# Performance work log

Measured on AMD Instinct MI355X. Metric: run time of the kernel, lower is better.

## Reference

```python
import jax, jax.numpy as jnp
import numpy as np

NUM_HEAD = 12
DIM_MODEL = 768
HEAD_DIM = DIM_MODEL // NUM_HEAD


def setup_inputs() -> dict:
    key = jax.random.key(0)
    ks = jax.random.split(key, 4)
    B, S, D = 2, 2048, DIM_MODEL
    scale = 1.0 / np.sqrt(D)
    return {
        "v1": jax.random.normal(ks[0], (B, S, D), dtype=jnp.float32),
        "v1_mask": jnp.zeros((B, 1, 1, S), dtype=jnp.float32),
        "Wq": jax.random.normal(ks[1], (D, D), dtype=jnp.float32) * scale,
        "bq": jnp.zeros((D,), dtype=jnp.float32),
        "Wk": jax.random.normal(ks[2], (D, D), dtype=jnp.float32) * scale,
        "bk": jnp.zeros((D,), dtype=jnp.float32),
        "Wv": jax.random.normal(ks[3], (D, D), dtype=jnp.float32) * scale,
        "bv": jnp.zeros((D,), dtype=jnp.float32),
    }


def reference(v1, v1_mask, Wq, bq, Wk, bk, Wv, bv):
    B, S, D = v1.shape
    H, hd = NUM_HEAD, HEAD_DIM

    def split_heads(x):  # [B,S,D] -> [B,H,S,hd]
        return x.reshape(B, S, H, hd).transpose(0, 2, 1, 3)

    q = split_heads(v1 @ Wq + bq)
    k = split_heads(v1 @ Wk + bk)
    v = split_heads(v1 @ Wv + bv)

    scores = jnp.einsum("bhqd,bhkd->bhqk", q, k) / jnp.sqrt(jnp.float32(hd))
    scores = scores + v1_mask  # additive mask broadcasts over heads/query
    probs = jax.nn.softmax(scores, axis=-1)
    # dropout is identity in eval/reference mode
    ctx = jnp.einsum("bhqk,bhkd->bhqd", probs, v)
    return ctx.transpose(0, 2, 1, 3).reshape(B, S, D)
```

## Files before the change

kernel.cpp:

```cpp
#include <hip/hip_runtime.h>
#include <math.h>

#define B_SZ 2
#define S_SZ 2048
#define D_SZ 768
#define NH   12
#define HD   64
#define BH_T (B_SZ * NH)
#define M_TOT (B_SZ * S_SZ)

using bfrag = __attribute__((ext_vector_type(8))) short;
using ffrag = __attribute__((ext_vector_type(4))) float;

__device__ __forceinline__ unsigned short f2bf(float f) {
    unsigned int u = __float_as_uint(f);
    u += 0x7fffu + ((u >> 16) & 1u);
    return (unsigned short)(u >> 16);
}
__device__ __forceinline__ unsigned short f2bf_fast(float f) {
    return (unsigned short)((__float_as_uint(f) + 0x8000u) >> 16);
}

__device__ __forceinline__ void async16(void* lds, const void* gp) {
    __builtin_amdgcn_global_load_lds(
        (const __attribute__((address_space(1))) unsigned int*)gp,
        (__attribute__((address_space(3))) unsigned int*)lds,
        16, 0, 0);
}

__global__ __launch_bounds__(256) void cvt_v1(const float* __restrict__ in,
                                              unsigned short* __restrict__ out) {
    int i = (blockIdx.x * 256 + threadIdx.x) * 4;
    float4 v = *(const float4*)&in[i];
    ushort4 o;
    o.x = f2bf(v.x); o.y = f2bf(v.y); o.z = f2bf(v.z); o.w = f2bf(v.w);
    *(ushort4*)&out[i] = o;
}

__global__ __launch_bounds__(256) void transpose_w(
    const float* __restrict__ Wq, const float* __restrict__ Wk,
    const float* __restrict__ Wv, unsigned short* __restrict__ Wt) {
    const int z = blockIdx.z;
    const float* W = (z == 0) ? Wq : (z == 1) ? Wk : Wv;
    unsigned short* dst = Wt + (size_t)z * D_SZ * D_SZ;
    __shared__ float tile[64][65];
    const int t = threadIdx.x;
    const int n0 = blockIdx.x * 64, k0 = blockIdx.y * 64;
    #pragma unroll
    for (int i = 0; i < 16; ++i) {
        int flat = i * 256 + t;
        int r = flat >> 6, c = flat & 63;
        tile[r][c] = W[(size_t)(k0 + r) * D_SZ + n0 + c];
    }
    __syncthreads();
    #pragma unroll
    for (int i = 0; i < 16; ++i) {
        int flat = i * 256 + t;
        int r = flat >> 6, c = flat & 63;
        dst[(size_t)(n0 + r) * D_SZ + k0 + c] = f2bf(tile[c][r]);
    }
}

#define CP_LD 136

__global__ __launch_bounds__(256) void proj_gemm(
    const unsigned short* __restrict__ Ab,
    const unsigned short* __restrict__ Wt,
    const float* __restrict__ bq, const float* __restrict__ bk_,
    const float* __restrict__ bv_,
    unsigned short* __restrict__ Qb, unsigned short* __restrict__ Kb,
    unsigned short* __restrict__ Vtb) {
    const int z = blockIdx.z;
    const unsigned short* Bt = Wt + (size_t)z * D_SZ * D_SZ;
    const float* bias = (z == 0) ? bq : (z == 1) ? bk_ : bv_;

    __shared__ unsigned short smem[128 * CP_LD];
    unsigned short* As = smem;
    unsigned short* Bs = smem + 128 * 64;

    const int t = threadIdx.x;
    const int lane = t & 63;
    const int w = t >> 6;
    const int wm = w & 1, wn = w >> 1;
    const int col = lane & 15;
    const int quad = lane >> 4;
    const int m0 = blockIdx.y * 128;
    const int n0 = blockIdx.x * 128;
    const int wbase = t & ~63;

    ffrag acc[4][4];
    #pragma unroll
    for (int i = 0; i < 4; ++i)
        #pragma unroll
        for (int j = 0; j < 4; ++j) { ffrag zf = {0.f, 0.f, 0.f, 0.f}; acc[i][j] = zf; }

    for (int k0 = 0; k0 < D_SZ; k0 += 64) {
        __syncthreads();
        #pragma unroll
        for (int i = 0; i < 4; ++i) {
            int c = i * 256 + t;
            int row = c >> 3;
            int gcol = ((c & 7) ^ (row & 7)) * 8;
            async16(&As[(size_t)(i * 256 + wbase) * 8],
                    &Ab[(size_t)(m0 + row) * D_SZ + k0 + gcol]);
        }
        #pragma unroll
        for (int i = 0; i < 4; ++i) {
            int c = i * 256 + t;
            int row = c >> 3;
            int gcol = ((c & 7) ^ (row & 7)) * 8;
            async16(&Bs[(size_t)(i * 256 + wbase) * 8],
                    &Bt[(size_t)(n0 + row) * D_SZ + k0 + gcol]);
        }
        __syncthreads();
        #pragma unroll
        for (int kk = 0; kk < 64; kk += 32) {
            const int cc = (kk >> 3) + quad;
            bfrag a[4], b[4];
            #pragma unroll
            for (int mi = 0; mi < 4; ++mi) {
                int row = wm * 64 + mi * 16 + col;
                a[mi] = *(const bfrag*)&As[row * 64 + ((cc ^ (row & 7)) * 8)];
            }
            #pragma unroll
            for (int ni = 0; ni < 4; ++ni) {
                int row = wn * 64 + ni * 16 + col;
                b[ni] = *(const bfrag*)&Bs[row * 64 + ((cc ^ (row & 7)) * 8)];
            }
            if (z == 2) {
                #pragma unroll
                for (int mi = 0; mi < 4; ++mi)
                    #pragma unroll
                    for (int ni = 0; ni < 4; ++ni)
                        acc[mi][ni] = __builtin_amdgcn_mfma_f32_16x16x32_bf16(
                            a[mi], b[ni], acc[mi][ni], 0, 0, 0);
            } else {
                #pragma unroll
                for (int mi = 0; mi < 4; ++mi)
                    #pragma unroll
                    for (int ni = 0; ni < 4; ++ni)
                        acc[mi][ni] = __builtin_amdgcn_mfma_f32_16x16x32_bf16(
                            b[ni], a[mi], acc[mi][ni], 0, 0, 0);
            }
        }
    }

    __syncthreads();

    if (z < 2) {
        const float sc = (z == 0) ? 0.125f : 1.0f;
        #pragma unroll
        for (int mi = 0; mi < 4; ++mi) {
            int m_local = wm * 64 + mi * 16 + col;
            #pragma unroll
            for (int ni = 0; ni < 4; ++ni) {
                int n_base = wn * 64 + ni * 16 + quad * 4;
                float4 b4 = *(const float4*)&bias[n0 + n_base];
                uint2 pk;
                pk.x = (unsigned)f2bf((acc[mi][ni][0] + b4.x) * sc) |
                       ((unsigned)f2bf((acc[mi][ni][1] + b4.y) * sc) << 16);
                pk.y = (unsigned)f2bf((acc[mi][ni][2] + b4.z) * sc) |
                       ((unsigned)f2bf((acc[mi][ni][3] + b4.w) * sc) << 16);
                *(uint2*)&smem[m_local * CP_LD + n_base] = pk;
            }
        }
        __syncthreads();
        unsigned short* Out = (z == 0) ? Qb : Kb;
        #pragma unroll
        for (int j = 0; j < 8; ++j) {
            int flat = j * 256 + t;
            int row = flat >> 4;
            int ch = flat & 15;
            uint4 vv = *(const uint4*)&smem[row * CP_LD + ch * 8];
            int m = m0 + row;
            int bb = m >> 11, s = m & 2047;
            int h = (n0 >> 6) + (ch >> 3);
            int d = (ch & 7) * 8;
            *(uint4*)&Out[((size_t)(bb * NH + h) * S_SZ + s) * HD + d] = vv;
        }
    } else {
        #pragma unroll
        for (int ni = 0; ni < 4; ++ni) {
            int n_local = wn * 64 + ni * 16 + col;
            float bvv = bias[n0 + n_local];
            #pragma unroll
            for (int mi = 0; mi < 4; ++mi) {
                int m_base = wm * 64 + mi * 16 + quad * 4;
                uint2 pk;
                pk.x = (unsigned)f2bf(acc[mi][ni][0] + bvv) |
                       ((unsigned)f2bf(acc[mi][ni][1] + bvv) << 16);
                pk.y = (unsigned)f2bf(acc[mi][ni][2] + bvv) |
                       ((unsigned)f2bf(acc[mi][ni][3] + bvv) << 16);
                *(uint2*)&smem[n_local * CP_LD + m_base] = pk;
            }
        }
        __syncthreads();
        #pragma unroll
        for (int j = 0; j < 8; ++j) {
            int flat = j * 256 + t;
            int row = flat >> 4;
            int ch = flat & 15;
            uint4 vv = *(const uint4*)&smem[row * CP_LD + ch * 8];
            int n = n0 + row;
            int h = n >> 6, d = n & 63;
            int m = m0 + ch * 8;
            int bb = m >> 11, s = m & 2047;
            *(uint4*)&Vtb[((size_t)(bb * NH + h) * HD + d) * S_SZ + s] = vv;
        }
    }
}

__global__ __launch_bounds__(256) void attn_mfma(
    const unsigned short* __restrict__ Qb, const unsigned short* __restrict__ Kb,
    const unsigned short* __restrict__ Vt, const float* __restrict__ mask,
    float* __restrict__ O0, float* __restrict__ O1, float* __restrict__ lp) {
    __shared__ unsigned short Ks[64 * 64];
    __shared__ unsigned short Vs[64 * 64];
    __shared__ unsigned short Ps[4][16 * 64];
    __shared__ float ms[64];

    const int t = threadIdx.x;
    const int lane = t & 63;
    const int w = t >> 6;
    const int col = lane & 15;
    const int quad = lane >> 4;
    const int q0 = blockIdx.x * 64;
    const int bh = blockIdx.y;
    const int split = blockIdx.z;
    const int b = bh / NH, h = bh % NH;
    const int wbase = t & ~63;

    const unsigned short* Qg = Qb + (size_t)bh * S_SZ * HD;
    const unsigned short* Kg = Kb + (size_t)bh * S_SZ * HD;
    const unsigned short* Vg = Vt + (size_t)bh * S_SZ * HD;
    const float* mrow = mask + (size_t)b * S_SZ;

    #pragma unroll
    for (int i = 0; i < 2; ++i) {
        int c = i * 256 + t;
        int row = c >> 3;
        int gcol = ((c & 7) ^ (row & 7)) * 8;
        async16(&Ks[(size_t)(i * 256 + wbase) * 8],
                &Qg[(size_t)(q0 + row) * HD + gcol]);
    }
    __syncthreads();
    const int arow = w * 16 + col;
    bfrag aq[2];
    #pragma unroll
    for (int kk = 0; kk < 2; ++kk) {
        int cc = kk * 4 + quad;
        aq[kk] = *(const bfrag*)&Ks[arow * 64 + ((cc ^ (arow & 7)) * 8)];
    }

    ffrag o[4];
    #pragma unroll
    for (int i = 0; i < 4; ++i) { ffrag zf = {0.f, 0.f, 0.f, 0.f}; o[i] = zf; }
    float lsum[4] = {0.f, 0.f, 0.f, 0.f};

    const int kbeg = split * (S_SZ / 2);
    for (int k0 = kbeg; k0 < kbeg + S_SZ / 2; k0 += 64) {
        __syncthreads();
        #pragma unroll
        for (int i = 0; i < 2; ++i) {
            int c = i * 256 + t;
            int row = c >> 3;
            int gcol = ((c & 7) ^ (row & 7)) * 8;
            async16(&Ks[(size_t)(i * 256 + wbase) * 8],
                    &Kg[(size_t)(k0 + row) * HD + gcol]);
            async16(&Vs[(size_t)(i * 256 + wbase) * 8],
                    &Vg[(size_t)row * S_SZ + k0 + gcol]);
        }
        if (t < 16) async16(&ms[0], &mrow[k0 + t * 4]);
        __syncthreads();

        ffrag s[4];
        #pragma unroll
        for (int i = 0; i < 4; ++i) { ffrag zf = {0.f, 0.f, 0.f, 0.f}; s[i] = zf; }
        #pragma unroll
        for (int kk = 0; kk < 2; ++kk) {
            const int cc = kk * 4 + quad;
            #pragma unroll
            for (int ni = 0; ni < 4; ++ni) {
                int brow = ni * 16 + col;
                bfrag bk8 = *(const bfrag*)&Ks[brow * 64 + ((cc ^ (brow & 7)) * 8)];
                s[ni] = __builtin_amdgcn_mfma_f32_16x16x32_bf16(aq[kk], bk8, s[ni], 0, 0, 0);
            }
        }

        #pragma unroll
        for (int ni = 0; ni < 4; ++ni) {
            float mv = ms[ni * 16 + col];
            #pragma unroll
            for (int r = 0; r < 4; ++r) {
                float e = __expf(s[ni][r] + mv);
                s[ni][r] = e;
                lsum[r] += e;
            }
        }

        unsigned short* Pw = &Ps[w][0];
        #pragma unroll
        for (int ni = 0; ni < 4; ++ni) {
            #pragma unroll
            for (int r = 0; r < 4; ++r) {
                int prow = quad * 4 + r;
                int pcol = ni * 16 + col;
                Pw[prow * 64 + (((pcol >> 3) ^ (prow & 7)) * 8) + (pcol & 7)] =
                    f2bf_fast(s[ni][r]);
            }
        }
        #pragma unroll
        for (int kk = 0; kk < 2; ++kk) {
            const int cc = kk * 4 + quad;
            bfrag ap = *(const bfrag*)&Pw[col * 64 + ((cc ^ (col & 7)) * 8)];
            #pragma unroll
            for (int di = 0; di < 4; ++di) {
                int vrow = di * 16 + col;
                bfrag bv8 = *(const bfrag*)&Vs[vrow * 64 + ((cc ^ (vrow & 7)) * 8)];
                o[di] = __builtin_amdgcn_mfma_f32_16x16x32_bf16(ap, bv8, o[di], 0, 0, 0);
            }
        }
    }

    #pragma unroll
    for (int r = 0; r < 4; ++r) {
        #pragma unroll
        for (int off = 1; off < 16; off <<= 1)
            lsum[r] += __shfl_xor(lsum[r], off);
    }

    float* Optr = (split == 0) ? O0 : O1;
    #pragma unroll
    for (int di = 0; di < 4; ++di) {
        int d = di * 16 + col;
        #pragma unroll
        for (int r = 0; r < 4; ++r) {
            int q = q0 + w * 16 + quad * 4 + r;
            Optr[((size_t)(b * S_SZ + q)) * D_SZ + h * HD + d] = o[di][r];
        }
    }
    if (col == 0) {
        #pragma unroll
        for (int r = 0; r < 4; ++r) {
            int q = q0 + w * 16 + quad * 4 + r;
            lp[((size_t)(split * B_SZ + b) * NH + h) * S_SZ + q] = lsum[r];
        }
    }
}

__global__ __launch_bounds__(256) void combine(
    float* __restrict__ out, const float* __restrict__ O1,
    const float* __restrict__ lp) {
    int i4 = blockIdx.x * 256 + threadIdx.x;
    int flat = i4 * 4;
    int b = flat / (S_SZ * D_SZ);
    int rem = flat % (S_SZ * D_SZ);
    int q = rem / D_SZ;
    int c = rem % D_SZ;
    int h = c >> 6;
    size_t l0i = ((size_t)b * NH + h) * S_SZ + q;
    float l = lp[l0i] + lp[(size_t)B_SZ * NH * S_SZ + l0i];
    float inv = 1.0f / l;
    float4 a = *(const float4*)&out[flat];
    float4 p = *(const float4*)&O1[flat];
    float4 r;
    r.x = (a.x + p.x) * inv;
    r.y = (a.y + p.y) * inv;
    r.z = (a.z + p.z) * inv;
    r.w = (a.w + p.w) * inv;
    *(float4*)&out[flat] = r;
}

extern "C" void kernel_launch(void* const* d_in, const int* in_sizes, int n_in,
                              void* d_out, int out_size, void* d_ws, size_t ws_size,
                              hipStream_t stream) {
    const float* v1   = (const float*)d_in[0];
    const float* mask = (const float*)d_in[1];
    const float* Wq   = (const float*)d_in[2];
    const float* bq   = (const float*)d_in[3];
    const float* Wk   = (const float*)d_in[4];
    const float* bk   = (const float*)d_in[5];
    const float* Wv   = (const float*)d_in[6];
    const float* bv   = (const float*)d_in[7];
    float* out = (float*)d_out;

    char* ws = (char*)d_ws;
    const size_t per_b = (size_t)BH_T * S_SZ * HD * 2;
    unsigned short* Qb  = (unsigned short*)(ws);
    unsigned short* Kb  = (unsigned short*)(ws + per_b);
    unsigned short* Vtb = (unsigned short*)(ws + 2 * per_b);
    unsigned short* v1b = (unsigned short*)(ws + 3 * per_b);
    unsigned short* Wt  = (unsigned short*)(ws + 3 * per_b + (size_t)M_TOT * D_SZ * 2);
    float* O1 = (float*)(ws + 3 * per_b);
    float* lp = (float*)(ws + 3 * per_b + (size_t)M_TOT * D_SZ * 4);

    cvt_v1<<<dim3((M_TOT * D_SZ) / 1024), 256, 0, stream>>>(v1, v1b);
    transpose_w<<<dim3(12, 12, 3), 256, 0, stream>>>(Wq, Wk, Wv, Wt);
    proj_gemm<<<dim3(6, 32, 3), 256, 0, stream>>>(v1b, Wt, bq, bk, bv, Qb, Kb, Vtb);
    attn_mfma<<<dim3(32, 24, 2), 256, 0, stream>>>(Qb, Kb, Vtb, mask, out, O1, lp);
    combine<<<dim3((M_TOT * D_SZ) / 1024), 256, 0, stream>>>(out, O1, lp);
}
```

Measured before the change: 168.4 us.

## Fuse split-K attention combine into one 512-thread block and merge prep kernels

The attention kernel now runs both key-halves inside a single 512-thread block, two groups of four waves each, and reduces them through LDS. This removes the separate combine kernel and the global round-trip of the partial O and row sums. The v1 conversion and weight transpose are merged into one prep launch. The projection GEMM M tile is halved to 64 to double the block count. The trade-off is fewer attention blocks with larger LDS use, plus an extra epilogue sync.

```diff
diff --git a/kernel.cpp b/kernel.cpp
--- a/kernel.cpp
+++ b/kernel.cpp
@@ -28,40 +28,45 @@
         16, 0, 0);
 }
 
-__global__ __launch_bounds__(256) void cvt_v1(const float* __restrict__ in,
-                                              unsigned short* __restrict__ out) {
-    int i = (blockIdx.x * 256 + threadIdx.x) * 4;
-    float4 v = *(const float4*)&in[i];
-    ushort4 o;
-    o.x = f2bf(v.x); o.y = f2bf(v.y); o.z = f2bf(v.z); o.w = f2bf(v.w);
-    *(ushort4*)&out[i] = o;
-}
-
-__global__ __launch_bounds__(256) void transpose_w(
+__global__ __launch_bounds__(256) void prep(
+    const float* __restrict__ v1,
     const float* __restrict__ Wq, const float* __restrict__ Wk,
-    const float* __restrict__ Wv, unsigned short* __restrict__ Wt) {
-    const int z = blockIdx.z;
-    const float* W = (z == 0) ? Wq : (z == 1) ? Wk : Wv;
-    unsigned short* dst = Wt + (size_t)z * D_SZ * D_SZ;
+    const float* __restrict__ Wv,
+    unsigned short* __restrict__ v1b, unsigned short* __restrict__ Wt) {
     __shared__ float tile[64][65];
+    const int bx = blockIdx.x;
     const int t = threadIdx.x;
-    const int n0 = blockIdx.x * 64, k0 = blockIdx.y * 64;
-    #pragma unroll
-    for (int i = 0; i < 16; ++i) {
-        int flat = i * 256 + t;
-        int r = flat >> 6, c = flat & 63;
-        tile[r][c] = W[(size_t)(k0 + r) * D_SZ + n0 + c];
-    }
-    __syncthreads();
-    #pragma unroll
-    for (int i = 0; i < 16; ++i) {
-        int flat = i * 256 + t;
-        int r = flat >> 6, c = flat & 63;
-        dst[(size_t)(n0 + r) * D_SZ + k0 + c] = f2bf(tile[c][r]);
+    if (bx < 3072) {
+        int i = (bx * 256 + t) * 4;
+        float4 v = *(const float4*)&v1[i];
+        ushort4 o;
+        o.x = f2bf(v.x); o.y = f2bf(v.y); o.z = f2bf(v.z); o.w = f2bf(v.w);
+        *(ushort4*)&v1b[i] = o;
+    } else {
+        int r = bx - 3072;
+        int z = r / 144;
+        int rr = r % 144;
+        int n0 = (rr % 12) * 64, k0 = (rr / 12) * 64;
+        const float* W = (z == 0) ? Wq : (z == 1) ? Wk : Wv;
+        unsigned short* dst = Wt + (size_t)z * D_SZ * D_SZ;
+        #pragma unroll
+        for (int i = 0; i < 16; ++i) {
+            int flat = i * 256 + t;
+            int rr2 = flat >> 6, c = flat & 63;
+            tile[rr2][c] = W[(size_t)(k0 + rr2) * D_SZ + n0 + c];
+        }
+        __syncthreads();
+        #pragma unroll
+        for (int i = 0; i < 16; ++i) {
+            int flat = i * 256 + t;
+            int rr2 = flat >> 6, c = flat & 63;
+            dst[(size_t)(n0 + rr2) * D_SZ + k0 + c] = f2bf(tile[c][rr2]);
+        }
     }
 }
 
 #define CP_LD 136
+#define CPV_LD 72
 
 __global__ __launch_bounds__(256) void proj_gemm(
     const unsigned short* __restrict__ Ab,
@@ -74,9 +79,9 @@
     const unsigned short* Bt = Wt + (size_t)z * D_SZ * D_SZ;
     const float* bias = (z == 0) ? bq : (z == 1) ? bk_ : bv_;
 
-    __shared__ unsigned short smem[128 * CP_LD];
+    __shared__ unsigned short smem[64 * 64 + 128 * 64];
     unsigned short* As = smem;
-    unsigned short* Bs = smem + 128 * 64;
+    unsigned short* Bs = smem + 64 * 64;
 
     const int t = threadIdx.x;
     const int lane = t & 63;
@@ -84,20 +89,20 @@
     const int wm = w & 1, wn = w >> 1;
     const int col = lane & 15;
     const int quad = lane >> 4;
-    const int m0 = blockIdx.y * 128;
+    const int m0 = blockIdx.y * 64;
     const int n0 = blockIdx.x * 128;
     const int wbase = t & ~63;
 
-    ffrag acc[4][4];
+    ffrag acc[2][4];
     #pragma unroll
-    for (int i = 0; i < 4; ++i)
+    for (int i = 0; i < 2; ++i)
         #pragma unroll
         for (int j = 0; j < 4; ++j) { ffrag zf = {0.f, 0.f, 0.f, 0.f}; acc[i][j] = zf; }
 
     for (int k0 = 0; k0 < D_SZ; k0 += 64) {
         __syncthreads();
         #pragma unroll
-        for (int i = 0; i < 4; ++i) {
+        for (int i = 0; i < 2; ++i) {
             int c = i * 256 + t;
             int row = c >> 3;
             int gcol = ((c & 7) ^ (row & 7)) * 8;
@@ -116,10 +121,10 @@
         #pragma unroll
         for (int kk = 0; kk < 64; kk += 32) {
             const int cc = (kk >> 3) + quad;
-            bfrag a[4], b[4];
-            #pragma unroll
-            for (int mi = 0; mi < 4; ++mi) {
-                int row = wm * 64 + mi * 16 + col;
+            bfrag a[2], b[4];
+            #pragma unroll
+            for (int mi = 0; mi < 2; ++mi) {
+                int row = wm * 32 + mi * 16 + col;
                 a[mi] = *(const bfrag*)&As[row * 64 + ((cc ^ (row & 7)) * 8)];
             }
             #pragma unroll
@@ -129,14 +134,14 @@
             }
             if (z == 2) {
                 #pragma unroll
-                for (int mi = 0; mi < 4; ++mi)
+                for (int mi = 0; mi < 2; ++mi)
                     #pragma unroll
                     for (int ni = 0; ni < 4; ++ni)
                         acc[mi][ni] = __builtin_amdgcn_mfma_f32_16x16x32_bf16(
                             a[mi], b[ni], acc[mi][ni], 0, 0, 0);
             } else {
                 #pragma unroll
-                for (int mi = 0; mi < 4; ++mi)
+                for (int mi = 0; mi < 2; ++mi)
                     #pragma unroll
                     for (int ni = 0; ni < 4; ++ni)
                         acc[mi][ni] = __builtin_amdgcn_mfma_f32_16x16x32_bf16(
@@ -150,8 +155,8 @@
     if (z < 2) {
         const float sc = (z == 0) ? 0.125f : 1.0f;
         #pragma unroll
-        for (int mi = 0; mi < 4; ++mi) {
-            int m_local = wm * 64 + mi * 16 + col;
+        for (int mi = 0; mi < 2; ++mi) {
+            int m_local = wm * 32 + mi * 16 + col;
             #pragma unroll
             for (int ni = 0; ni < 4; ++ni) {
                 int n_base = wn * 64 + ni * 16 + quad * 4;
@@ -167,7 +172,7 @@
         __syncthreads();
         unsigned short* Out = (z == 0) ? Qb : Kb;
         #pragma unroll
-        for (int j = 0; j < 8; ++j) {
+        for (int j = 0; j < 4; ++j) {
             int flat = j * 256 + t;
             int row = flat >> 4;
             int ch = flat & 15;
@@ -184,23 +189,23 @@
             int n_local = wn * 64 + ni * 16 + col;
             float bvv = bias[n0 + n_local];
             #pragma unroll
-            for (int mi = 0; mi < 4; ++mi) {
-                int m_base = wm * 64 + mi * 16 + quad * 4;
+            for (int mi = 0; mi < 2; ++mi) {
+                int m_base = wm * 32 + mi * 16 + quad * 4;
                 uint2 pk;
                 pk.x = (unsigned)f2bf(acc[mi][ni][0] + bvv) |
                        ((unsigned)f2bf(acc[mi][ni][1] + bvv) << 16);
                 pk.y = (unsigned)f2bf(acc[mi][ni][2] + bvv) |
                        ((unsigned)f2bf(acc[mi][ni][3] + bvv) << 16);
-                *(uint2*)&smem[n_local * CP_LD + m_base] = pk;
-            }
-        }
-        __syncthreads();
-        #pragma unroll
-        for (int j = 0; j < 8; ++j) {
+                *(uint2*)&smem[n_local * CPV_LD + m_base] = pk;
+            }
+        }
+        __syncthreads();
+        #pragma unroll
+        for (int j = 0; j < 4; ++j) {
             int flat = j * 256 + t;
-            int row = flat >> 4;
-            int ch = flat & 15;
-            uint4 vv = *(const uint4*)&smem[row * CP_LD + ch * 8];
+            int row = flat >> 3;
+            int ch = flat & 7;
+            uint4 vv = *(const uint4*)&smem[row * CPV_LD + ch * 8];
             int n = n0 + row;
             int h = n >> 6, d = n & 63;
             int m = m0 + ch * 8;
@@ -210,46 +215,48 @@
     }
 }
 
-__global__ __launch_bounds__(256) void attn_mfma(
+__global__ __launch_bounds__(512) void attn_mfma(
     const unsigned short* __restrict__ Qb, const unsigned short* __restrict__ Kb,
     const unsigned short* __restrict__ Vt, const float* __restrict__ mask,
-    float* __restrict__ O0, float* __restrict__ O1, float* __restrict__ lp) {
-    __shared__ unsigned short Ks[64 * 64];
-    __shared__ unsigned short Vs[64 * 64];
-    __shared__ unsigned short Ps[4][16 * 64];
-    __shared__ float ms[64];
+    float* __restrict__ out) {
+    __shared__ union {
+        unsigned short stage[2][2][64 * 64];
+        struct { float Of[64][68]; float ls1[64]; } ep;
+    } u;
+    __shared__ unsigned short Ps[8][16 * 64];
+    __shared__ float ms[2][64];
 
     const int t = threadIdx.x;
     const int lane = t & 63;
     const int w = t >> 6;
+    const int g = w >> 2;
+    const int wq = w & 3;
+    const int tg = t & 255;
     const int col = lane & 15;
     const int quad = lane >> 4;
     const int q0 = blockIdx.x * 64;
     const int bh = blockIdx.y;
-    const int split = blockIdx.z;
     const int b = bh / NH, h = bh % NH;
-    const int wbase = t & ~63;
+    const int wbase = tg & ~63;
 
     const unsigned short* Qg = Qb + (size_t)bh * S_SZ * HD;
     const unsigned short* Kg = Kb + (size_t)bh * S_SZ * HD;
     const unsigned short* Vg = Vt + (size_t)bh * S_SZ * HD;
     const float* mrow = mask + (size_t)b * S_SZ;
 
-    #pragma unroll
-    for (int i = 0; i < 2; ++i) {
-        int c = i * 256 + t;
-        int row = c >> 3;
-        int gcol = ((c & 7) ^ (row & 7)) * 8;
-        async16(&Ks[(size_t)(i * 256 + wbase) * 8],
+    {
+        int row = t >> 3;
+        int gcol = ((t & 7) ^ (row & 7)) * 8;
+        async16(&u.stage[0][0][(size_t)(t & ~63) * 8],
                 &Qg[(size_t)(q0 + row) * HD + gcol]);
     }
     __syncthreads();
-    const int arow = w * 16 + col;
+    const int arow = wq * 16 + col;
     bfrag aq[2];
     #pragma unroll
     for (int kk = 0; kk < 2; ++kk) {
         int cc = kk * 4 + quad;
-        aq[kk] = *(const bfrag*)&Ks[arow * 64 + ((cc ^ (arow & 7)) * 8)];
+        aq[kk] = *(const bfrag*)&u.stage[0][0][arow * 64 + ((cc ^ (arow & 7)) * 8)];
     }
 
     ffrag o[4];
@@ -257,21 +264,24 @@
     for (int i = 0; i < 4; ++i) { ffrag zf = {0.f, 0.f, 0.f, 0.f}; o[i] = zf; }
     float lsum[4] = {0.f, 0.f, 0.f, 0.f};
 
-    const int kbeg = split * (S_SZ / 2);
+    const int kbeg = g * (S_SZ / 2);
     for (int k0 = kbeg; k0 < kbeg + S_SZ / 2; k0 += 64) {
         __syncthreads();
         #pragma unroll
         for (int i = 0; i < 2; ++i) {
-            int c = i * 256 + t;
+            int c = i * 256 + tg;
             int row = c >> 3;
             int gcol = ((c & 7) ^ (row & 7)) * 8;
-            async16(&Ks[(size_t)(i * 256 + wbase) * 8],
+            async16(&u.stage[0][g][(size_t)(i * 256 + wbase) * 8],
                     &Kg[(size_t)(k0 + row) * HD + gcol]);
-            async16(&Vs[(size_t)(i * 256 + wbase) * 8],
+            async16(&u.stage[1][g][(size_t)(i * 256 + wbase) * 8],
                     &Vg[(size_t)row * S_SZ + k0 + gcol]);
         }
-        if (t < 16) async16(&ms[0], &mrow[k0 + t * 4]);
-        __syncthreads();
+        if (tg < 16) async16(&ms[g][0], &mrow[k0 + tg * 4]);
+        __syncthreads();
+
+        const unsigned short* Ks = u.stage[0][g];
+        const unsigned short* Vs = u.stage[1][g];
 
         ffrag s[4];
         #pragma unroll
@@ -289,7 +299,7 @@
 
         #pragma unroll
         for (int ni = 0; ni < 4; ++ni) {
-            float mv = ms[ni * 16 + col];
+            float mv = ms[g][ni * 16 + col];
             #pragma unroll
             for (int r = 0; r < 4; ++r) {
                 float e = __expf(s[ni][r] + mv);
@@ -329,46 +339,40 @@
             lsum[r] += __shfl_xor(lsum[r], off);
     }
 
-    float* Optr = (split == 0) ? O0 : O1;
-    #pragma unroll
-    for (int di = 0; di < 4; ++di) {
-        int d = di * 16 + col;
+    __syncthreads();
+    if (g == 1) {
+        #pragma unroll
+        for (int di = 0; di < 4; ++di) {
+            int d = di * 16 + col;
+            #pragma unroll
+            for (int r = 0; r < 4; ++r)
+                u.ep.Of[wq * 16 + quad * 4 + r][d] = o[di][r];
+        }
+        if (col == 0) {
+            #pragma unroll
+            for (int r = 0; r < 4; ++r)
+                u.ep.ls1[wq * 16 + quad * 4 + r] = lsum[r];
+        }
+    }
+    __syncthreads();
+    if (g == 0) {
+        float inv[4];
         #pragma unroll
         for (int r = 0; r < 4; ++r) {
-            int q = q0 + w * 16 + quad * 4 + r;
-            Optr[((size_t)(b * S_SZ + q)) * D_SZ + h * HD + d] = o[di][r];
-        }
-    }
-    if (col == 0) {
-        #pragma unroll
-        for (int r = 0; r < 4; ++r) {
-            int q = q0 + w * 16 + quad * 4 + r;
-            lp[((size_t)(split * B_SZ + b) * NH + h) * S_SZ + q] = lsum[r];
-        }
-    }
-}
-
-__global__ __launch_bounds__(256) void combine(
-    float* __restrict__ out, const float* __restrict__ O1,
-    const float* __restrict__ lp) {
-    int i4 = blockIdx.x * 256 + threadIdx.x;
-    int flat = i4 * 4;
-    int b = flat / (S_SZ * D_SZ);
-    int rem = flat % (S_SZ * D_SZ);
-    int q = rem / D_SZ;
-    int c = rem % D_SZ;
-    int h = c >> 6;
-    size_t l0i = ((size_t)b * NH + h) * S_SZ + q;
-    float l = lp[l0i] + lp[(size_t)B_SZ * NH * S_SZ + l0i];
-    float inv = 1.0f / l;
-    float4 a = *(const float4*)&out[flat];
-    float4 p = *(const float4*)&O1[flat];
-    float4 r;
-    r.x = (a.x + p.x) * inv;
-    r.y = (a.y + p.y) * inv;
-    r.z = (a.z + p.z) * inv;
-    r.w = (a.w + p.w) * inv;
-    *(float4*)&out[flat] = r;
+            int qr = wq * 16 + quad * 4 + r;
+            inv[r] = 1.0f / (lsum[r] + u.ep.ls1[qr]);
+        }
+        #pragma unroll
+        for (int di = 0; di < 4; ++di) {
+            int d = di * 16 + col;
+            #pragma unroll
+            for (int r = 0; r < 4; ++r) {
+                int qr = wq * 16 + quad * 4 + r;
+                out[((size_t)(b * S_SZ + q0 + qr)) * D_SZ + h * HD + d] =
+                    (o[di][r] + u.ep.Of[qr][d]) * inv[r];
+            }
+        }
+    }
 }
 
 extern "C" void kernel_launch(void* const* d_in, const int* in_sizes, int n_in,
@@ -391,12 +395,8 @@
     unsigned short* Vtb = (unsigned short*)(ws + 2 * per_b);
     unsigned short* v1b = (unsigned short*)(ws + 3 * per_b);
     unsigned short* Wt  = (unsigned short*)(ws + 3 * per_b + (size_t)M_TOT * D_SZ * 2);
-    float* O1 = (float*)(ws + 3 * per_b);
-    float* lp = (float*)(ws + 3 * per_b + (size_t)M_TOT * D_SZ * 4);
-
-    cvt_v1<<<dim3((M_TOT * D_SZ) / 1024), 256, 0, stream>>>(v1, v1b);
-    transpose_w<<<dim3(12, 12, 3), 256, 0, stream>>>(Wq, Wk, Wv, Wt);
-    proj_gemm<<<dim3(6, 32, 3), 256, 0, stream>>>(v1b, Wt, bq, bk, bv, Qb, Kb, Vtb);
-    attn_mfma<<<dim3(32, 24, 2), 256, 0, stream>>>(Qb, Kb, Vtb, mask, out, O1, lp);
-    combine<<<dim3((M_TOT * D_SZ) / 1024), 256, 0, stream>>>(out, O1, lp);
-}
+
+    prep<<<dim3(3072 + 432), 256, 0, stream>>>(v1, Wq, Wk, Wv, v1b, Wt);
+    proj_gemm<<<dim3(6, 64, 3), 256, 0, stream>>>(v1b, Wt, bq, bk, bv, Qb, Kb, Vtb);
+    attn_mfma<<<dim3(32, 24), 512, 0, stream>>>(Qb, Kb, Vtb, mask, out);
+}
```

Result: faster. 160.2 us (-4.8%).
